# Performance work log

Measured on AMD Instinct MI355X. Metric: run time of the kernel, lower is better.

## Reference

```python
import jax, jax.numpy as jnp
import numpy as np

NUM_HEADS = 16
THRESHOLD = 0.1  # default forward arg; with seq_len > 2**max_qubits the Grover path degenerates to probs > threshold


def setup_inputs() -> dict:
    key = jax.random.key(0)
    ks = jax.random.split(key, 5)
    B, S, E = 4, 1024, 1024
    return {
        "x": jax.random.normal(ks[0], (B, S, E), dtype=jnp.float32),
        "w_qkv": jax.random.normal(ks[1], (E, 3 * E), dtype=jnp.float32) * (E ** -0.5),
        "b_qkv": jax.random.normal(ks[2], (3 * E,), dtype=jnp.float32) * 0.02,
        "w_proj": jax.random.normal(ks[3], (E, E), dtype=jnp.float32) * (E ** -0.5),
        "b_proj": jax.random.normal(ks[4], (E,), dtype=jnp.float32) * 0.02,
    }


def reference(x, w_qkv, b_qkv, w_proj, b_proj):
    B, S, E = x.shape
    H = NUM_HEADS
    Dh = E // H
    scale = Dh ** -0.5
    # qkv projection -> [3, B, H, S, Dh]
    qkv = (x @ w_qkv + b_qkv).reshape(B, S, 3, H, Dh).transpose(2, 0, 3, 1, 4)
    q, k, v = qkv[0], qkv[1], qkv[2]
    attn_logits = jnp.einsum("bhqd,bhkd->bhqk", q, k) * scale  # [B,H,S,S]
    attn_probs = jax.nn.softmax(attn_logits, axis=-1)
    # Grover filter degenerates to threshold mask for S > 2**max_qubits
    mask = attn_probs > THRESHOLD
    any_selected = jnp.any(mask, axis=-1, keepdims=True)
    # fallback: keep only the argmax column in rows where nothing passed threshold
    fallback = jax.nn.one_hot(jnp.argmax(attn_probs, axis=-1), S, dtype=jnp.bool_)
    mask = jnp.where(any_selected, mask, fallback)
    filtered_logits = jnp.where(mask, attn_logits, -jnp.inf)
    filtered_attn = jax.nn.softmax(filtered_logits, axis=-1)
    # dropout is identity in eval / p=0
    out = jnp.einsum("bhqk,bhkd->bhqd", filtered_attn, v)  # [B,H,S,Dh]
    out = out.transpose(0, 2, 1, 3).reshape(B, S, E)
    out = out @ w_proj + b_proj
    return out, filtered_attn
```

## Files before the change

kernel.cpp:

```cpp
#include <hip/hip_runtime.h>
#include <math.h>

#define SS 1024
#define OUT0_SZ (4*1024*1024)

typedef _Float16 f16;
typedef _Float16 h8 __attribute__((ext_vector_type(8)));
typedef _Float16 h4 __attribute__((ext_vector_type(4)));
typedef float f32x4 __attribute__((ext_vector_type(4)));

#define MFMA(a,b,c) __builtin_amdgcn_mfma_f32_16x16x32_f16(a, b, c, 0, 0, 0)

__device__ __forceinline__ void gload_lds16(const void* g, void* l) {
  __builtin_amdgcn_global_load_lds((const __attribute__((address_space(1))) void*)g,
                                   (__attribute__((address_space(3))) void*)l, 16, 0, 0);
}

template<int SPLIT>
__global__ __launch_bounds__(256)
void transpose_split(const float* __restrict__ in, f16* __restrict__ outHi,
                     f16* __restrict__ outLo, int K, int N, float scale) {
  __shared__ float t[32][33];
  const int n0 = blockIdx.x * 32, k0 = blockIdx.y * 32;
  const int tx = threadIdx.x & 31, ty = threadIdx.x >> 5;
#pragma unroll
  for (int j = 0; j < 4; j++)
    t[ty + j * 8][tx] = in[(size_t)(k0 + ty + j * 8) * N + n0 + tx] * scale;
  __syncthreads();
#pragma unroll
  for (int j = 0; j < 4; j++) {
    float v = t[tx][ty + j * 8];
    f16 h = (f16)v;
    size_t idx = (size_t)(n0 + ty + j * 8) * K + k0 + tx;
    outHi[idx] = h;
    if (SPLIT) outLo[idx] = (f16)(v - (float)h);
  }
}

__global__ __launch_bounds__(256)
void splitx(const float* __restrict__ x, f16* __restrict__ hi, f16* __restrict__ lo) {
  const size_t i4 = (size_t)blockIdx.x * 256 + threadIdx.x;
  float4 v = ((const float4*)x)[i4];
  float vv[4] = {v.x, v.y, v.z, v.w};
  h4 hh, ll;
#pragma unroll
  for (int j = 0; j < 4; j++) {
    float sv = vv[j] * 64.f;
    f16 h = (f16)sv;
    hh[j] = h; ll[j] = (f16)(sv - (float)h);
  }
  ((h4*)hi)[i4] = hh;
  ((h4*)lo)[i4] = ll;
}

__global__ __launch_bounds__(256)
void transpose_v(const f16* __restrict__ in, f16* __restrict__ out) {
  __shared__ f16 t[32][33];
  const int bh = blockIdx.z, s0 = blockIdx.x * 32, d0 = blockIdx.y * 32;
  in  += (size_t)bh * 65536;
  out += (size_t)bh * 65536;
  const int tx = threadIdx.x & 31, ty = threadIdx.x >> 5;
#pragma unroll
  for (int j = 0; j < 4; j++)
    t[ty + j * 8][tx] = in[(size_t)(s0 + ty + j * 8) * 64 + d0 + tx];
  __syncthreads();
#pragma unroll
  for (int j = 0; j < 4; j++)
    out[(size_t)(d0 + ty + j * 8) * 1024 + s0 + tx] = t[tx][ty + j * 8];
}

__global__ __launch_bounds__(256)
void qkv_gemm(const f16* __restrict__ Xhi, const f16* __restrict__ Xlo,
              const f16* __restrict__ WhiT, const f16* __restrict__ WloT,
              const float* __restrict__ bias,
              f16* __restrict__ Qhi, f16* __restrict__ Qlo,
              f16* __restrict__ Khi, f16* __restrict__ Klo, f16* __restrict__ Vf) {
  __shared__ __align__(16) f16 Ah[128 * 32], Al[128 * 32], Bh[128 * 32], Bl[128 * 32];
  const int tid = threadIdx.x, w = tid >> 6, l = tid & 63;
  const int n0 = blockIdx.x * 128, m0 = blockIdx.y * 128;
  const int wr = (w & 1) * 64, wc = (w >> 1) * 64;
  const int fr = l & 15, fq = l >> 4;
  f32x4 acc[4][4] = {};

  for (int kt = 0; kt < 1024; kt += 32) {
    __syncthreads();
#pragma unroll
    for (int i = 0; i < 2; i++) {
      int row = w * 32 + i * 16 + (l >> 2);
      int co = kt + (l & 3) * 8;
      size_t aoff = (size_t)(m0 + row) * 1024 + co;
      size_t boff = (size_t)(n0 + row) * 1024 + co;
      gload_lds16(Xhi  + aoff, Ah + w * 1024 + i * 512);
      gload_lds16(Xlo  + aoff, Al + w * 1024 + i * 512);
      gload_lds16(WhiT + boff, Bh + w * 1024 + i * 512);
      gload_lds16(WloT + boff, Bl + w * 1024 + i * 512);
    }
    __syncthreads();
    h8 ah[4], al[4], bh[4], bl[4];
#pragma unroll
    for (int m = 0; m < 4; m++) {
      ah[m] = *(h8*)&Ah[(wr + m * 16 + fr) * 32 + fq * 8];
      al[m] = *(h8*)&Al[(wr + m * 16 + fr) * 32 + fq * 8];
    }
#pragma unroll
    for (int n = 0; n < 4; n++) {
      bh[n] = *(h8*)&Bh[(wc + n * 16 + fr) * 32 + fq * 8];
      bl[n] = *(h8*)&Bl[(wc + n * 16 + fr) * 32 + fq * 8];
    }
#pragma unroll
    for (int m = 0; m < 4; m++)
#pragma unroll
      for (int n = 0; n < 4; n++) {
        acc[m][n] = MFMA(ah[m], bh[n], acc[m][n]);
        acc[m][n] = MFMA(al[m], bh[n], acc[m][n]);
        acc[m][n] = MFMA(ah[m], bl[n], acc[m][n]);
      }
  }

#pragma unroll
  for (int m = 0; m < 4; m++)
#pragma unroll
    for (int n = 0; n < 4; n++)
#pragma unroll
      for (int j = 0; j < 4; j++) {
        int row = m0 + wr + m * 16 + fq * 4 + j;
        int col = n0 + wc + n * 16 + fr;
        float val = acc[m][n][j] * (1.f / 262144.f) + bias[col];
        int t = col >> 10, h = (col >> 6) & 15, d = col & 63;
        int b = row >> 10, s = row & 1023;
        size_t idx = ((size_t)(b * 16 + h) * 1024 + s) * 64 + d;
        if (t == 0) { f16 hh = (f16)(val * 64.f); Qhi[idx] = hh; Qlo[idx] = (f16)(val * 64.f - (float)hh); }
        else if (t == 1) { f16 hh = (f16)(val * 64.f); Khi[idx] = hh; Klo[idx] = (f16)(val * 64.f - (float)hh); }
        else Vf[idx] = (f16)val;
      }
}

__global__ __launch_bounds__(256)
void qksm(const f16* __restrict__ Qhi, const f16* __restrict__ Qlo,
          const f16* __restrict__ Khi, const f16* __restrict__ Klo,
          float* __restrict__ att) {
  __shared__ float P[32][1028];
  __shared__ __align__(16) f16 KH[4096], KL[4096];
  const int bh = blockIdx.y, m0 = blockIdx.x * 32;
  const size_t off = (size_t)bh * 65536;
  const int tid = threadIdx.x, w = tid >> 6, l = tid & 63;
  const int fr = l & 15, fq = l >> 4;
  const int nw = w * 16;

  h8 qh[2][2], ql[2][2];
#pragma unroll
  for (int m = 0; m < 2; m++)
#pragma unroll
    for (int kk = 0; kk < 2; kk++) {
      size_t o = off + (size_t)(m0 + 16 * m + fr) * 64 + kk * 32 + fq * 8;
      qh[m][kk] = *(const h8*)(Qhi + o);
      ql[m][kk] = *(const h8*)(Qlo + o);
    }

  const char* KhiB = (const char*)(Khi + off);
  const char* KloB = (const char*)(Klo + off);

  for (int c = 0; c < 16; c++) {
    {
      int i0 = w * 2;
#pragma unroll
      for (int i = i0; i < i0 + 2; i++) {
        int r = i * 8 + (l >> 3);
        size_t gb = (size_t)(c * 64 + r) * 128 + (size_t)(((l & 7) * 16) ^ ((r & 7) << 4));
        gload_lds16(KhiB + gb, (char*)KH + i * 1024);
        gload_lds16(KloB + gb, (char*)KL + i * 1024);
      }
    }
    __syncthreads();
    f32x4 acc[2] = {};
    const int R = nw + fr;
    const int rs = (R & 7) << 4;
#pragma unroll
    for (int kk = 0; kk < 2; kk++) {
      h8 b_h = *(const h8*)((const char*)KH + R * 128 + ((kk * 64 + fq * 16) ^ rs));
      h8 b_l = *(const h8*)((const char*)KL + R * 128 + ((kk * 64 + fq * 16) ^ rs));
#pragma unroll
      for (int m = 0; m < 2; m++) {
        acc[m] = MFMA(qh[m][kk], b_h, acc[m]);
        acc[m] = MFMA(ql[m][kk], b_h, acc[m]);
        acc[m] = MFMA(qh[m][kk], b_l, acc[m]);
      }
    }
#pragma unroll
    for (int m = 0; m < 2; m++)
#pragma unroll
      for (int j = 0; j < 4; j++)
        P[16 * m + fq * 4 + j][c * 64 + nw + fr] = acc[m][j] * (1.f / 32768.f);
    __syncthreads();
  }

  const int r0 = w * 8;
  for (int rr = 0; rr < 8; rr++) {
    const int r = r0 + rr;
    float z[16];
#pragma unroll
    for (int i = 0; i < 16; i++) z[i] = P[r][l + 64 * i];
    float m = z[0]; int am = l;
#pragma unroll
    for (int i = 1; i < 16; i++) { int idx = l + 64 * i; if (z[i] > m) { m = z[i]; am = idx; } }
#pragma unroll
    for (int o = 32; o >= 1; o >>= 1) {
      float om = __shfl_xor(m, o, 64);
      int oa = __shfl_xor(am, o, 64);
      if (om > m || (om == m && oa < am)) { m = om; am = oa; }
    }
    float e[16]; float s = 0.f;
#pragma unroll
    for (int i = 0; i < 16; i++) { e[i] = expf(z[i] - m); s += e[i]; }
#pragma unroll
    for (int o = 32; o >= 1; o >>= 1) s += __shfl_xor(s, o, 64);
    bool sel[16]; float fl = 0.f; int anyl = 0;
#pragma unroll
    for (int i = 0; i < 16; i++) {
      sel[i] = (e[i] / s > 0.1f);
      if (sel[i]) { fl += e[i]; anyl = 1; }
    }
#pragma unroll
    for (int o = 32; o >= 1; o >>= 1) fl += __shfl_xor(fl, o, 64);
    int any = __any(anyl);
    float* arow = att + ((size_t)bh << 20) + (size_t)(m0 + r) * 1024;
#pragma unroll
    for (int i = 0; i < 16; i++) {
      float v;
      if (any) v = sel[i] ? e[i] / fl : 0.f;
      else     v = ((l + 64 * i) == am) ? 1.f : 0.f;
      arow[l + 64 * i] = v;
    }
  }
}

__global__ __launch_bounds__(256)
void pv_gemm(const float* __restrict__ att, const f16* __restrict__ Vt,
             f16* __restrict__ ao) {
  __shared__ __align__(16) f16 A[128 * 32], B[64 * 32];
  const int bh = blockIdx.y, m0 = blockIdx.x * 128;
  const float* fa = att + (size_t)bh * 1048576;
  const f16* Vb = Vt + (size_t)bh * 65536;
  const int tid = threadIdx.x, w = tid >> 6, l = tid & 63;
  const int wr = (w & 1) * 64, wc = (w >> 1) * 32;
  const int fr = l & 15, fq = l >> 4;
  f32x4 acc[4][2] = {};

  for (int kt = 0; kt < 1024; kt += 32) {
    __syncthreads();
    {
      int row = w * 16 + (l >> 2);
      gload_lds16(Vb + (size_t)row * 1024 + kt + (l & 3) * 8, B + w * 512);
    }
#pragma unroll
    for (int r4 = 0; r4 < 4; r4++) {
      int f = r4 * 256 + tid;
      int row = f >> 3, c4 = (f & 7) * 4;
      float4 pv4 = *(const float4*)&fa[(size_t)(m0 + row) * 1024 + kt + c4];
      h4 hh;
      hh[0] = (f16)pv4.x; hh[1] = (f16)pv4.y; hh[2] = (f16)pv4.z; hh[3] = (f16)pv4.w;
      *(h4*)&A[row * 32 + c4] = hh;
    }
    __syncthreads();
    h8 a[4], b[2];
#pragma unroll
    for (int m = 0; m < 4; m++) a[m] = *(h8*)&A[(wr + m * 16 + fr) * 32 + fq * 8];
#pragma unroll
    for (int n = 0; n < 2; n++) b[n] = *(h8*)&B[(wc + n * 16 + fr) * 32 + fq * 8];
#pragma unroll
    for (int m = 0; m < 4; m++)
#pragma unroll
      for (int n = 0; n < 2; n++) acc[m][n] = MFMA(a[m], b[n], acc[m][n]);
  }

  const int b = bh >> 4, h = bh & 15;
#pragma unroll
  for (int m = 0; m < 4; m++)
#pragma unroll
    for (int n = 0; n < 2; n++)
#pragma unroll
      for (int j = 0; j < 4; j++) {
        int s = m0 + wr + m * 16 + fq * 4 + j;
        int d = wc + n * 16 + fr;
        ao[((size_t)(b * 1024 + s)) * 1024 + h * 64 + d] = (f16)acc[m][n][j];
      }
}

__global__ __launch_bounds__(256)
void proj_gemm(const f16* __restrict__ ao, const f16* __restrict__ WpT,
               const float* __restrict__ bias, float* __restrict__ out) {
  __shared__ __align__(16) f16 A[128 * 32], B[128 * 32];
  const int tid = threadIdx.x, w = tid >> 6, l = tid & 63;
  const int n0 = blockIdx.x * 128, m0 = blockIdx.y * 128;
  const int wr = (w & 1) * 64, wc = (w >> 1) * 64;
  const int fr = l & 15, fq = l >> 4;
  f32x4 acc[4][4] = {};

  for (int kt = 0; kt < 1024; kt += 32) {
    __syncthreads();
#pragma unroll
    for (int i = 0; i < 2; i++) {
      int row = w * 32 + i * 16 + (l >> 2);
      gload_lds16(ao  + (size_t)(m0 + row) * 1024 + kt + (l & 3) * 8, A + w * 1024 + i * 512);
      gload_lds16(WpT + (size_t)(n0 + row) * 1024 + kt + (l & 3) * 8, B + w * 1024 + i * 512);
    }
    __syncthreads();
    h8 a[4], b[4];
#pragma unroll
    for (int m = 0; m < 4; m++) a[m] = *(h8*)&A[(wr + m * 16 + fr) * 32 + fq * 8];
#pragma unroll
    for (int n = 0; n < 4; n++) b[n] = *(h8*)&B[(wc + n * 16 + fr) * 32 + fq * 8];
#pragma unroll
    for (int m = 0; m < 4; m++)
#pragma unroll
      for (int n = 0; n < 4; n++) acc[m][n] = MFMA(a[m], b[n], acc[m][n]);
  }

#pragma unroll
  for (int m = 0; m < 4; m++)
#pragma unroll
    for (int n = 0; n < 4; n++)
#pragma unroll
      for (int j = 0; j < 4; j++) {
        int row = m0 + wr + m * 16 + fq * 4 + j;
        int col = n0 + wc + n * 16 + fr;
        out[(size_t)row * 1024 + col] = acc[m][n][j] + bias[col];
      }
}

extern "C" void kernel_launch(void* const* d_in, const int* in_sizes, int n_in,
                              void* d_out, int out_size, void* d_ws, size_t ws_size,
                              hipStream_t stream) {
  const float* x      = (const float*)d_in[0];
  const float* w_qkv  = (const float*)d_in[1];
  const float* b_qkv  = (const float*)d_in[2];
  const float* w_proj = (const float*)d_in[3];
  const float* b_proj = (const float*)d_in[4];

  float* out0 = (float*)d_out;
  float* att  = out0 + OUT0_SZ;

  f16* Xhi = (f16*)att;
  f16* Xlo = Xhi + 4194304;

  f16* ws16 = (f16*)d_ws;
  f16* WhiT = ws16;
  f16* WloT = ws16 +  3145728;
  f16* WpT  = ws16 +  6291456;
  f16* Qhi  = ws16 +  7340032;
  f16* Qlo  = ws16 + 11534336;
  f16* Khi  = ws16 + 15728640;
  f16* Klo  = ws16 + 19922944;
  f16* Vf   = ws16 + 24117248;
  f16* Vt   = ws16 + 28311552;
  f16* ao16 = ws16;

  transpose_split<1><<<dim3(96, 32), 256, 0, stream>>>(w_qkv, WhiT, WloT, 1024, 3072, 4096.f);
  transpose_split<0><<<dim3(32, 32), 256, 0, stream>>>(w_proj, WpT, nullptr, 1024, 1024, 1.f);
  splitx<<<4096, 256, 0, stream>>>(x, Xhi, Xlo);
  qkv_gemm<<<dim3(24, 32), 256, 0, stream>>>(Xhi, Xlo, WhiT, WloT, b_qkv, Qhi, Qlo, Khi, Klo, Vf);
  transpose_v<<<dim3(32, 2, 64), 256, 0, stream>>>(Vf, Vt);
  qksm<<<dim3(32, 64), 256, 0, stream>>>(Qhi, Qlo, Khi, Klo, att);
  pv_gemm<<<dim3(8, 64), 256, 0, stream>>>(att, Vt, ao16);
  proj_gemm<<<dim3(8, 32), 256, 0, stream>>>(ao16, WpT, b_proj, out0);
}
```

Measured before the change: 727.0 us.

## Halve qksm row tile and read K directly from global, dropping LDS staging

The QK-softmax kernel now handles 16 query rows per block instead of 32, doubling the grid. It drops the LDS staging of K tiles and the per-chunk barriers, loading K fragments straight from global memory into MFMA operands. The P buffer shrinks from about 131KB to 64KB, which should allow more blocks per CU and remove barrier stalls. In exchange, K is re-read from global/L2 twice as often, with uncoalesced 16-byte per-lane loads.

```diff
diff --git a/kernel.cpp b/kernel.cpp
--- a/kernel.cpp
+++ b/kernel.cpp
@@ -139,64 +139,41 @@
 void qksm(const f16* __restrict__ Qhi, const f16* __restrict__ Qlo,
           const f16* __restrict__ Khi, const f16* __restrict__ Klo,
           float* __restrict__ att) {
-  __shared__ float P[32][1028];
-  __shared__ __align__(16) f16 KH[4096], KL[4096];
-  const int bh = blockIdx.y, m0 = blockIdx.x * 32;
+  __shared__ float P[16][1024];
+  const int bh = blockIdx.y, m0 = blockIdx.x * 16;
   const size_t off = (size_t)bh * 65536;
   const int tid = threadIdx.x, w = tid >> 6, l = tid & 63;
   const int fr = l & 15, fq = l >> 4;
   const int nw = w * 16;
 
-  h8 qh[2][2], ql[2][2];
-#pragma unroll
-  for (int m = 0; m < 2; m++)
+  h8 qh[2], ql[2];
+#pragma unroll
+  for (int kk = 0; kk < 2; kk++) {
+    size_t o = off + (size_t)(m0 + fr) * 64 + kk * 32 + fq * 8;
+    qh[kk] = *(const h8*)(Qhi + o);
+    ql[kk] = *(const h8*)(Qlo + o);
+  }
+
+  for (int c = 0; c < 16; c++) {
+    f32x4 acc = {};
+    const int krow = c * 64 + nw + fr;
 #pragma unroll
     for (int kk = 0; kk < 2; kk++) {
-      size_t o = off + (size_t)(m0 + 16 * m + fr) * 64 + kk * 32 + fq * 8;
-      qh[m][kk] = *(const h8*)(Qhi + o);
-      ql[m][kk] = *(const h8*)(Qlo + o);
-    }
-
-  const char* KhiB = (const char*)(Khi + off);
-  const char* KloB = (const char*)(Klo + off);
-
-  for (int c = 0; c < 16; c++) {
-    {
-      int i0 = w * 2;
-#pragma unroll
-      for (int i = i0; i < i0 + 2; i++) {
-        int r = i * 8 + (l >> 3);
-        size_t gb = (size_t)(c * 64 + r) * 128 + (size_t)(((l & 7) * 16) ^ ((r & 7) << 4));
-        gload_lds16(KhiB + gb, (char*)KH + i * 1024);
-        gload_lds16(KloB + gb, (char*)KL + i * 1024);
-      }
-    }
-    __syncthreads();
-    f32x4 acc[2] = {};
-    const int R = nw + fr;
-    const int rs = (R & 7) << 4;
-#pragma unroll
-    for (int kk = 0; kk < 2; kk++) {
-      h8 b_h = *(const h8*)((const char*)KH + R * 128 + ((kk * 64 + fq * 16) ^ rs));
-      h8 b_l = *(const h8*)((const char*)KL + R * 128 + ((kk * 64 + fq * 16) ^ rs));
-#pragma unroll
-      for (int m = 0; m < 2; m++) {
-        acc[m] = MFMA(qh[m][kk], b_h, acc[m]);
-        acc[m] = MFMA(ql[m][kk], b_h, acc[m]);
-        acc[m] = MFMA(qh[m][kk], b_l, acc[m]);
-      }
-    }
-#pragma unroll
-    for (int m = 0; m < 2; m++)
-#pragma unroll
-      for (int j = 0; j < 4; j++)
-        P[16 * m + fq * 4 + j][c * 64 + nw + fr] = acc[m][j] * (1.f / 32768.f);
-    __syncthreads();
-  }
-
-  const int r0 = w * 8;
-  for (int rr = 0; rr < 8; rr++) {
-    const int r = r0 + rr;
+      size_t o = off + (size_t)krow * 64 + kk * 32 + fq * 8;
+      h8 b_h = *(const h8*)(Khi + o);
+      h8 b_l = *(const h8*)(Klo + o);
+      acc = MFMA(qh[kk], b_h, acc);
+      acc = MFMA(ql[kk], b_h, acc);
+      acc = MFMA(qh[kk], b_l, acc);
+    }
+#pragma unroll
+    for (int j = 0; j < 4; j++)
+      P[fq * 4 + j][c * 64 + nw + fr] = acc[j] * (1.f / 32768.f);
+  }
+  __syncthreads();
+
+  for (int rr = 0; rr < 4; rr++) {
+    const int r = w * 4 + rr;
     float z[16];
 #pragma unroll
     for (int i = 0; i < 16; i++) z[i] = P[r][l + 64 * i];
@@ -360,7 +337,7 @@
   splitx<<<4096, 256, 0, stream>>>(x, Xhi, Xlo);
   qkv_gemm<<<dim3(24, 32), 256, 0, stream>>>(Xhi, Xlo, WhiT, WloT, b_qkv, Qhi, Qlo, Khi, Klo, Vf);
   transpose_v<<<dim3(32, 2, 64), 256, 0, stream>>>(Vf, Vt);
-  qksm<<<dim3(32, 64), 256, 0, stream>>>(Qhi, Qlo, Khi, Klo, att);
+  qksm<<<dim3(64, 64), 256, 0, stream>>>(Qhi, Qlo, Khi, Klo, att);
   pv_gemm<<<dim3(8, 64), 256, 0, stream>>>(att, Vt, ao16);
   proj_gemm<<<dim3(8, 32), 256, 0, stream>>>(ao16, WpT, b_proj, out0);
 }
```

After: 651.2 us. -10.4%, faster.
